# Kernel optimization log

Measured on AMD Instinct MI355X. Metric: run time of the kernel, lower is better.

## Reference

```python
import jax, jax.numpy as jnp
import numpy as np

C = 1024
H = 16
DH = C // H
DFF = 4 * C
D = 1024  # cond_dim
B = 2
L = 2048
MAX_SCALE_MUL = float(np.log(100.0))
EPS = 1e-6


def _ln(x):
    # LayerNorm without affine, eps=1e-6
    m = jnp.mean(x, axis=-1, keepdims=True)
    xc = x - m
    var = jnp.mean(xc * xc, axis=-1, keepdims=True)
    return xc * jax.lax.rsqrt(var + EPS)


def setup_inputs() -> dict:
    key = jax.random.key(0)
    ks = jax.random.split(key, 16)
    s = 0.02
    return {
        "x": jax.random.normal(ks[0], (B, L, C), jnp.float32),
        "cond_BD": jax.random.normal(ks[1], (B, D), jnp.float32),
        "attn_bias": jax.random.normal(ks[2], (1, 1, L, L), jnp.float32) * 0.1,
        "qkv_w": jax.random.normal(ks[3], (3 * C, C), jnp.float32) * s,
        "q_bias": jnp.zeros((C,), jnp.float32),
        "v_bias": jnp.zeros((C,), jnp.float32),
        "scale_mul": jnp.full((1, H, 1, 1), np.log(4.0), jnp.float32),
        "proj_w": jax.random.normal(ks[4], (C, C), jnp.float32) * s,
        "proj_b": jnp.zeros((C,), jnp.float32),
        "fc1_w": jax.random.normal(ks[5], (DFF, C), jnp.float32) * s,
        "fc1_b": jnp.zeros((DFF,), jnp.float32),
        "fc2_w": jax.random.normal(ks[6], (C, DFF), jnp.float32) * s,
        "fc2_b": jnp.zeros((C,), jnp.float32),
        "ada_w": jax.random.normal(ks[7], (6 * C, D), jnp.float32) * s,
        "ada_b": jnp.zeros((6 * C,), jnp.float32),
    }


def _attention(x, attn_bias, qkv_w, q_bias, v_bias, scale_mul, proj_w, proj_b):
    b, l, c = x.shape
    bias = jnp.concatenate([q_bias, jnp.zeros_like(q_bias), v_bias])
    qkv = x @ qkv_w.T + bias  # [B,L,3C]
    qkv = qkv.reshape(b, l, 3, H, DH).transpose(2, 0, 3, 1, 4)  # [3,B,H,L,DH]
    q, k, v = qkv[0], qkv[1], qkv[2]
    sm = jnp.exp(jnp.minimum(scale_mul, MAX_SCALE_MUL))  # [1,H,1,1]
    q = q * jax.lax.rsqrt(jnp.sum(q * q, -1, keepdims=True).clip(1e-24)) * sm
    k = k * jax.lax.rsqrt(jnp.sum(k * k, -1, keepdims=True).clip(1e-24))
    attn = jnp.einsum("bhqd,bhkd->bhqk", q, k) + attn_bias
    attn = jax.nn.softmax(attn, axis=-1)
    out = jnp.einsum("bhqk,bhkd->bhqd", attn, v)
    out = out.transpose(0, 2, 1, 3).reshape(b, l, c)
    return out @ proj_w.T + proj_b


def reference(x, cond_BD, attn_bias, qkv_w, q_bias, v_bias, scale_mul,
              proj_w, proj_b, fc1_w, fc1_b, fc2_w, fc2_b, ada_w, ada_b):
    # adaLN modulation: SiLU -> Linear -> 6 chunks of C
    ada = jax.nn.silu(cond_BD) @ ada_w.T + ada_b  # [B,6C]
    ada = ada.reshape(-1, 1, 6, C)
    g1, g2, s1, s2, sh1, sh2 = [ada[:, :, i, :] for i in range(6)]  # each [B,1,C]
    # attention branch
    h = _ln(x) * (s1 + 1.0) + sh1
    x = x + _attention(h, attn_bias, qkv_w, q_bias, v_bias, scale_mul, proj_w, proj_b) * g1
    # FFN branch (GELU tanh approx)
    h = _ln(x) * (s2 + 1.0) + sh2
    h = jax.nn.gelu(h @ fc1_w.T + fc1_b, approximate=True) @ fc2_w.T + fc2_b
    x = x + h * g2
    return x
```

## Files before the change

kernel.cpp:

```cpp
#include <hip/hip_runtime.h>
#include <stdint.h>

#define Ll 2048
#define Mrows 4096

typedef unsigned short u16;
typedef __attribute__((ext_vector_type(8))) short short8;
typedef __attribute__((ext_vector_type(4))) float f32x4;

__device__ __forceinline__ float b2f(u16 b) {
  union { float f; unsigned u; } x; x.u = ((unsigned)b) << 16; return x.f;
}
__device__ __forceinline__ u16 f2b(float v) {
  union { float f; unsigned u; } x; x.f = v;
  unsigned r = x.u + 0x7fffu + ((x.u >> 16) & 1u);
  return (u16)(r >> 16);
}

#define GLOAD_LDS16(gp, sp)                                                        \
  __builtin_amdgcn_global_load_lds(                                                \
      (__attribute__((address_space(1))) void*)(void*)(gp),                        \
      (__attribute__((address_space(3))) void*)(sp), 16, 0, 0)

__global__ __launch_bounds__(256) void k_f32_to_bf16(const float* __restrict__ src,
                                                     u16* __restrict__ dst) {
  const int i = blockIdx.x * 256 + threadIdx.x;
  const float4 v = ((const float4*)src)[i];
  ushort4 o;
  o.x = f2b(v.x); o.y = f2b(v.y); o.z = f2b(v.z); o.w = f2b(v.w);
  ((ushort4*)dst)[i] = o;
}

__global__ void k_qkvbias(const float* __restrict__ qb, const float* __restrict__ vb,
                          float* __restrict__ out) {
  const int i = blockIdx.x * 256 + threadIdx.x;
  out[i] = (i < 1024) ? qb[i] : (i < 2048 ? 0.f : vb[i - 2048]);
}

__global__ __launch_bounds__(256) void k_ada(const float* __restrict__ cond,
                                             const float* __restrict__ aw,
                                             const float* __restrict__ ab,
                                             float* __restrict__ out) {
  const int wv = threadIdx.x >> 6, lane = threadIdx.x & 63;
  const int j = blockIdx.x * 4 + wv;
  const int b = j / 6144, jj = j % 6144;
  const float* wr = aw + (size_t)jj * 1024;
  const float* cr = cond + b * 1024;
  float acc = 0.f;
  for (int d = lane; d < 1024; d += 64) {
    const float cv = cr[d];
    acc += (cv / (1.f + __expf(-cv))) * wr[d];
  }
  for (int off = 32; off; off >>= 1) acc += __shfl_xor(acc, off);
  if (lane == 0) out[b * 6144 + jj] = acc + ab[jj];
}

__global__ __launch_bounds__(256) void k_ln_mod(const float* __restrict__ x,
                                                const float* __restrict__ ada,
                                                u16* __restrict__ out,
                                                int s_off, int sh_off) {
  const int row = blockIdx.x;
  const int b = row >> 11;
  const int t = threadIdx.x;
  const float4 xv = ((const float4*)(x + (size_t)row * 1024))[t];
  float s = xv.x + xv.y + xv.z + xv.w;
  float s2 = xv.x * xv.x + xv.y * xv.y + xv.z * xv.z + xv.w * xv.w;
  for (int off = 32; off; off >>= 1) { s += __shfl_xor(s, off); s2 += __shfl_xor(s2, off); }
  __shared__ float red[8];
  const int wv = t >> 6, lane = t & 63;
  if (lane == 0) { red[wv] = s; red[4 + wv] = s2; }
  __syncthreads();
  s = red[0] + red[1] + red[2] + red[3];
  s2 = red[4] + red[5] + red[6] + red[7];
  const float mean = s * (1.f / 1024.f);
  const float var = s2 * (1.f / 1024.f) - mean * mean;
  const float rstd = rsqrtf(var + 1e-6f);
  const float4 sv = ((const float4*)(ada + b * 6144 + s_off))[t];
  const float4 shv = ((const float4*)(ada + b * 6144 + sh_off))[t];
  ushort4 ov;
  ov.x = f2b((xv.x - mean) * rstd * (1.f + sv.x) + shv.x);
  ov.y = f2b((xv.y - mean) * rstd * (1.f + sv.y) + shv.y);
  ov.z = f2b((xv.z - mean) * rstd * (1.f + sv.z) + shv.z);
  ov.w = f2b((xv.w - mean) * rstd * (1.f + sv.w) + shv.w);
  ((ushort4*)(out + (size_t)row * 1024))[t] = ov;
}

__global__ __launch_bounds__(256) void k_resid_ln(const float* __restrict__ x,
                                                  const float* __restrict__ p,
                                                  const float* __restrict__ ada,
                                                  float* __restrict__ x2,
                                                  u16* __restrict__ out) {
  const int row = blockIdx.x;
  const int b = row >> 11;
  const int t = threadIdx.x;
  const float4 xv = ((const float4*)(x + (size_t)row * 1024))[t];
  const float4 pv = ((const float4*)(p + (size_t)row * 1024))[t];
  const float4 gv = ((const float4*)(ada + b * 6144 + 0))[t];
  float4 v;
  v.x = xv.x + pv.x * gv.x; v.y = xv.y + pv.y * gv.y;
  v.z = xv.z + pv.z * gv.z; v.w = xv.w + pv.w * gv.w;
  ((float4*)(x2 + (size_t)row * 1024))[t] = v;
  float s = v.x + v.y + v.z + v.w;
  float s2 = v.x * v.x + v.y * v.y + v.z * v.z + v.w * v.w;
  for (int off = 32; off; off >>= 1) { s += __shfl_xor(s, off); s2 += __shfl_xor(s2, off); }
  __shared__ float red[8];
  const int wv = t >> 6, lane = t & 63;
  if (lane == 0) { red[wv] = s; red[4 + wv] = s2; }
  __syncthreads();
  s = red[0] + red[1] + red[2] + red[3];
  s2 = red[4] + red[5] + red[6] + red[7];
  const float mean = s * (1.f / 1024.f);
  const float var = s2 * (1.f / 1024.f) - mean * mean;
  const float rstd = rsqrtf(var + 1e-6f);
  const float4 sv = ((const float4*)(ada + b * 6144 + 3072))[t];
  const float4 shv = ((const float4*)(ada + b * 6144 + 5120))[t];
  ushort4 ov;
  ov.x = f2b((v.x - mean) * rstd * (1.f + sv.x) + shv.x);
  ov.y = f2b((v.y - mean) * rstd * (1.f + sv.y) + shv.y);
  ov.z = f2b((v.z - mean) * rstd * (1.f + sv.z) + shv.z);
  ov.w = f2b((v.w - mean) * rstd * (1.f + sv.w) + shv.w);
  ((ushort4*)(out + (size_t)row * 1024))[t] = ov;
}

__global__ __launch_bounds__(256) void k_final(const float* __restrict__ x2,
                                               const float* __restrict__ f,
                                               const float* __restrict__ ada,
                                               float* __restrict__ out) {
  const int i = blockIdx.x * 256 + threadIdx.x;
  const int elem = i * 4;
  const int b = elem >> 21;
  const int c = elem & 1023;
  const float4 xv = ((const float4*)x2)[i];
  const float4 fv = ((const float4*)f)[i];
  const float4 gv = *(const float4*)(ada + b * 6144 + 1024 + c);
  float4 ov;
  ov.x = xv.x + fv.x * gv.x; ov.y = xv.y + fv.y * gv.y;
  ov.z = xv.z + fv.z * gv.z; ov.w = xv.w + fv.w * gv.w;
  ((float4*)out)[i] = ov;
}

__global__ __launch_bounds__(256) void k_qknorm(u16* __restrict__ qkv,
                                                const float* __restrict__ scale_mul) {
  const int wv = threadIdx.x >> 6, lane = threadIdx.x & 63;
  const int item = blockIdx.x * 4 + wv;
  const int h = item & 15;
  const int bl = item >> 4;
  const size_t base = (size_t)bl * 3072 + h * 64;
  const float q = b2f(qkv[base + lane]);
  float ss = q * q;
  for (int off = 32; off; off >>= 1) ss += __shfl_xor(ss, off);
  const float sm = __expf(fminf(scale_mul[h], 4.605170185988091f));
  qkv[base + lane] = f2b(q * rsqrtf(fmaxf(ss, 1e-24f)) * sm);
  const float k = b2f(qkv[base + 1024 + lane]);
  ss = k * k;
  for (int off = 32; off; off >>= 1) ss += __shfl_xor(ss, off);
  qkv[base + 1024 + lane] = f2b(k * rsqrtf(fmaxf(ss, 1e-24f)));
}

template <int OUT_BF16, int GELU_ACT>
__global__ __launch_bounds__(256, 2)
void k_gemm_bt(const u16* __restrict__ A, const u16* __restrict__ W,
               const float* __restrict__ bias, void* __restrict__ Cout,
               int M, int N, int K) {
  __shared__ u16 As[128 * 64];
  __shared__ u16 Bs[128 * 64];
  const int tid = threadIdx.x;
  const int wv = tid >> 6;
  const int lane = tid & 63;
  const int q = lane >> 4;
  const int r = lane & 15;
  const int wm = (wv & 1) * 64;
  const int wn = (wv >> 1) * 64;
  const int m0 = blockIdx.x * 128;
  const int n0 = blockIdx.y * 128;

  f32x4 acc[4][4];
#pragma unroll
  for (int i = 0; i < 4; ++i)
#pragma unroll
    for (int j = 0; j < 4; ++j) acc[i][j] = (f32x4)0.0f;

  const int srow = tid >> 3;
  const int scol = (tid & 7) * 8;
  const u16* Ag = A + (size_t)(m0 + srow) * K + scol;
  const u16* Wg = W + (size_t)(n0 + srow) * K + scol;
  u16* AsBase = &As[wv * 512];
  u16* BsBase = &Bs[wv * 512];

  for (int kt = 0; kt < K; kt += 64) {
    __syncthreads();
#pragma unroll
    for (int p = 0; p < 4; ++p) {
      GLOAD_LDS16(Ag + (size_t)(p * 32) * K + kt, AsBase + p * 2048);
      GLOAD_LDS16(Wg + (size_t)(p * 32) * K + kt, BsBase + p * 2048);
    }
    __syncthreads();
#pragma unroll
    for (int kc = 0; kc < 2; ++kc) {
      short8 af[4], bfr[4];
#pragma unroll
      for (int i = 0; i < 4; ++i) {
        af[i] = *(const short8*)(As + (wm + i * 16 + r) * 64 + kc * 32 + q * 8);
        bfr[i] = *(const short8*)(Bs + (wn + i * 16 + r) * 64 + kc * 32 + q * 8);
      }
#pragma unroll
      for (int mi = 0; mi < 4; ++mi)
#pragma unroll
        for (int ni = 0; ni < 4; ++ni)
          acc[mi][ni] = __builtin_amdgcn_mfma_f32_16x16x32_bf16(af[mi], bfr[ni],
                                                                acc[mi][ni], 0, 0, 0);
    }
  }
#pragma unroll
  for (int mi = 0; mi < 4; ++mi) {
#pragma unroll
    for (int ni = 0; ni < 4; ++ni) {
      const int col = n0 + wn + ni * 16 + r;
      const float bv = bias[col];
#pragma unroll
      for (int rr = 0; rr < 4; ++rr) {
        const int rowg = m0 + wm + mi * 16 + q * 4 + rr;
        float v = acc[mi][ni][rr] + bv;
        if (GELU_ACT) {
          const float t = tanhf(0.7978845608028654f * (v + 0.044715f * v * v * v));
          v = 0.5f * v * (1.0f + t);
        }
        if (OUT_BF16)
          ((u16*)Cout)[(size_t)rowg * N + col] = f2b(v);
        else
          ((float*)Cout)[(size_t)rowg * N + col] = v;
      }
    }
  }
}

__global__ __launch_bounds__(256)
void k_flash(const u16* __restrict__ qkv, const u16* __restrict__ bias16,
             const float* __restrict__ scale_mul, u16* __restrict__ o) {
  __shared__ u16 Qs[64 * 64];
  __shared__ u16 Ks[64 * 64];
  __shared__ u16 Vt[64 * 72];
  __shared__ u16 Ps[4][16 * 64];
  __shared__ float stat[4][16];
  const int tid = threadIdx.x;
  const int bh = blockIdx.x;
  const int qb = blockIdx.y;
  const int b = bh >> 4, h = bh & 15;
  const int wv = tid >> 6, lane = tid & 63;
  const int quad = lane >> 4, c = lane & 15;
  const u16* Qg = qkv + (size_t)b * Ll * 3072 + h * 64;
  const u16* Kg = Qg + 1024;
  const u16* Vg = Qg + 2048;
  const float FMAX = __expf(fminf(scale_mul[h], 4.605170185988091f)) + 1.0f;

  {
    const int srow = tid >> 3, scol = (tid & 7) * 8;
    const u16* gp = Qg + (size_t)(qb * 64 + srow) * 3072 + scol;
    u16* lp = &Qs[wv * 512];
    GLOAD_LDS16(gp, lp);
    GLOAD_LDS16(gp + (size_t)32 * 3072, lp + 2048);
  }

  const int vc = tid & 15, va = (tid >> 4) & 1, vd0 = (tid >> 5) * 8;

  f32x4 S[4], O[4];
  float lacc[4];
#pragma unroll
  for (int i = 0; i < 4; ++i) { O[i] = (f32x4)0.f; lacc[i] = 0.f; }
  const u16* brow = bias16 + (size_t)(qb * 64 + wv * 16 + quad * 4) * 2048;

  for (int kt = 0; kt < 32; ++kt) {
    __syncthreads();
    {
      const int srow = tid >> 3, scol = (tid & 7) * 8;
      const u16* gp = Kg + (size_t)(kt * 64 + srow) * 3072 + scol;
      u16* lp = &Ks[wv * 512];
      GLOAD_LDS16(gp, lp);
      GLOAD_LDS16(gp + (size_t)32 * 3072, lp + 2048);
    }
    {
      union { uint4 v; u16 s[8]; } r0, r1;
      const u16* vp = Vg + (size_t)(kt * 64 + vc + 32 * va) * 3072 + vd0;
      r0.v = *(const uint4*)vp;
      r1.v = *(const uint4*)(vp + (size_t)16 * 3072);
#pragma unroll
      for (int j = 0; j < 8; ++j)
        *(unsigned*)(&Vt[(vd0 + j) * 72 + vc * 4 + va * 2]) =
            (unsigned)r0.s[j] | ((unsigned)r1.s[j] << 16);
    }
    __syncthreads();

    u16 bv[4][4];
#pragma unroll
    for (int rr = 0; rr < 4; ++rr)
#pragma unroll
      for (int ni = 0; ni < 4; ++ni)
        bv[rr][ni] = brow[rr * 2048 + kt * 64 + ni * 16 + c];

#pragma unroll
    for (int i = 0; i < 4; ++i) S[i] = (f32x4)0.f;
#pragma unroll
    for (int ks = 0; ks < 2; ++ks) {
      const short8 aq = *(const short8*)(&Qs[(wv * 16 + c) * 64 + ks * 32 + quad * 8]);
#pragma unroll
      for (int ni = 0; ni < 4; ++ni) {
        const short8 bk = *(const short8*)(&Ks[(ni * 16 + c) * 64 + ks * 32 + quad * 8]);
        S[ni] = __builtin_amdgcn_mfma_f32_16x16x32_bf16(aq, bk, S[ni], 0, 0, 0);
      }
    }

#pragma unroll
    for (int rr = 0; rr < 4; ++rr) {
      const float p0 = __expf(S[0][rr] + b2f(bv[rr][0]) - FMAX);
      const float p1 = __expf(S[1][rr] + b2f(bv[rr][1]) - FMAX);
      const float p2 = __expf(S[2][rr] + b2f(bv[rr][2]) - FMAX);
      const float p3 = __expf(S[3][rr] + b2f(bv[rr][3]) - FMAX);
      lacc[rr] += (p0 + p1) + (p2 + p3);
      ushort4 pk;
      pk.x = f2b(p0); pk.y = f2b(p1); pk.z = f2b(p2); pk.w = f2b(p3);
      *(ushort4*)(&Ps[wv][(quad * 4 + rr) * 64 + c * 4]) = pk;
    }
    __threadfence_block();
#pragma unroll
    for (int ks = 0; ks < 2; ++ks) {
      const short8 bp = *(const short8*)(&Ps[wv][c * 64 + ks * 32 + quad * 8]);
#pragma unroll
      for (int i = 0; i < 4; ++i) {
        const short8 av = *(const short8*)(&Vt[(i * 16 + c) * 72 + ks * 32 + quad * 8]);
        O[i] = __builtin_amdgcn_mfma_f32_16x16x32_bf16(av, bp, O[i], 0, 0, 0);
      }
    }
  }

#pragma unroll
  for (int rr = 0; rr < 4; ++rr) {
    float l = lacc[rr];
    l += __shfl_xor(l, 1); l += __shfl_xor(l, 2);
    l += __shfl_xor(l, 4); l += __shfl_xor(l, 8);
    lacc[rr] = l;
  }
  if (c == 0)
    *(float4*)(&stat[wv][quad * 4]) = make_float4(lacc[0], lacc[1], lacc[2], lacc[3]);
  __threadfence_block();
  const float inv = 1.f / stat[wv][c];
  u16* op = o + (size_t)(b * Ll + qb * 64 + wv * 16 + c) * 1024 + h * 64;
#pragma unroll
  for (int i = 0; i < 4; ++i) {
    ushort4 ov;
    ov.x = f2b(O[i][0] * inv); ov.y = f2b(O[i][1] * inv);
    ov.z = f2b(O[i][2] * inv); ov.w = f2b(O[i][3] * inv);
    *(ushort4*)(op + i * 16 + quad * 4) = ov;
  }
}

extern "C" void kernel_launch(void* const* d_in, const int* in_sizes, int n_in,
                              void* d_out, int out_size, void* d_ws, size_t ws_size,
                              hipStream_t stream) {
  const float* x = (const float*)d_in[0];
  const float* cond = (const float*)d_in[1];
  const float* attn_bias = (const float*)d_in[2];
  const float* qkv_w = (const float*)d_in[3];
  const float* q_bias = (const float*)d_in[4];
  const float* v_bias = (const float*)d_in[5];
  const float* scale_mul = (const float*)d_in[6];
  const float* proj_w = (const float*)d_in[7];
  const float* proj_b = (const float*)d_in[8];
  const float* fc1_w = (const float*)d_in[9];
  const float* fc1_b = (const float*)d_in[10];
  const float* fc2_w = (const float*)d_in[11];
  const float* fc2_b = (const float*)d_in[12];
  const float* ada_w = (const float*)d_in[13];
  const float* ada_b = (const float*)d_in[14];
  float* out = (float*)d_out;
  char* ws = (char*)d_ws;

  float* ada_out = (float*)(ws + 0);
  float* qkv_bias = (float*)(ws + 49152);
  u16* wqkv = (u16*)(ws + 61440);
  u16* wproj = (u16*)(ws + 6352896);
  u16* wfc1 = (u16*)(ws + 8450048);
  u16* wfc2 = (u16*)(ws + 16838656);
  u16* sb = (u16*)(ws + 25227264);
  u16* big = (u16*)(ws + 33615872);
  float* g32 = (float*)(ws + 67170304);
  float* x2 = (float*)(ws + 83947520);
  u16* wbias = big + (size_t)4096 * 3072;

  k_f32_to_bf16<<<3072, 256, 0, stream>>>(qkv_w, wqkv);
  k_f32_to_bf16<<<1024, 256, 0, stream>>>(proj_w, wproj);
  k_f32_to_bf16<<<4096, 256, 0, stream>>>(fc1_w, wfc1);
  k_f32_to_bf16<<<4096, 256, 0, stream>>>(fc2_w, wfc2);
  k_f32_to_bf16<<<4096, 256, 0, stream>>>(attn_bias, wbias);
  k_qkvbias<<<12, 256, 0, stream>>>(q_bias, v_bias, qkv_bias);
  k_ada<<<3072, 256, 0, stream>>>(cond, ada_w, ada_b, ada_out);
  k_ln_mod<<<4096, 256, 0, stream>>>(x, ada_out, sb, 2048, 4096);
  k_gemm_bt<1, 0><<<dim3(32, 24), 256, 0, stream>>>(sb, wqkv, qkv_bias, big,
                                                    Mrows, 3072, 1024);
  k_qknorm<<<16384, 256, 0, stream>>>(big, scale_mul);
  k_flash<<<dim3(32, 32), 256, 0, stream>>>(big, wbias, scale_mul, sb);
  k_gemm_bt<0, 0><<<dim3(32, 8), 256, 0, stream>>>(sb, wproj, proj_b, g32,
                                                   Mrows, 1024, 1024);
  k_resid_ln<<<4096, 256, 0, stream>>>(x, g32, ada_out, x2, sb);
  k_gemm_bt<1, 1><<<dim3(32, 32), 256, 0, stream>>>(sb, wfc1, fc1_b, big,
                                                    Mrows, 4096, 1024);
  k_gemm_bt<0, 0><<<dim3(32, 8), 256, 0, stream>>>(big, wfc2, fc2_b, g32,
                                                   Mrows, 1024, 4096);
  k_final<<<4096, 256, 0, stream>>>(x2, g32, ada_out, out);
}
```

Before: 514.4 us.

## Split-K the narrow GEMMs, fuse QK-norm into QKV GEMM, merge conversions

The proj and fc2 GEMMs (N=1024, 256 tiles) now use two-way split-K over gridDim.z. This raises the tile count to 512 so the CUs are better filled, and the two partial outputs are summed inside the residual/LN and final kernels. A dedicated QKV GEMM applies the q/v bias, the per-head L2 normalisation and the scale in its epilogue using intra-quad shuffles, removing the separate qknorm pass over the QKV buffer. The five weight/bias conversions become one kernel launch, and the qkv_bias kernel is dropped. In exchange, each split-K GEMM writes an extra fp32 partial buffer, which adds memory traffic, and workspace regions are reused for those partials.

```diff
diff --git a/kernel.cpp b/kernel.cpp
--- a/kernel.cpp
+++ b/kernel.cpp
@@ -22,19 +22,24 @@
       (__attribute__((address_space(1))) void*)(void*)(gp),                        \
       (__attribute__((address_space(3))) void*)(sp), 16, 0, 0)
 
-__global__ __launch_bounds__(256) void k_f32_to_bf16(const float* __restrict__ src,
-                                                     u16* __restrict__ dst) {
-  const int i = blockIdx.x * 256 + threadIdx.x;
-  const float4 v = ((const float4*)src)[i];
+__global__ __launch_bounds__(256) void k_convert_all(
+    const float* __restrict__ s0, u16* __restrict__ d0,
+    const float* __restrict__ s1, u16* __restrict__ d1,
+    const float* __restrict__ s2, u16* __restrict__ d2,
+    const float* __restrict__ s3, u16* __restrict__ d3,
+    const float* __restrict__ s4, u16* __restrict__ d4) {
+  int i = blockIdx.x * 256 + threadIdx.x;
+  const float* s; u16* d; int off;
+  if (i < 786432)       { s = s0; d = d0; off = 0; }
+  else if (i < 1048576) { s = s1; d = d1; off = 786432; }
+  else if (i < 2097152) { s = s2; d = d2; off = 1048576; }
+  else if (i < 3145728) { s = s3; d = d3; off = 2097152; }
+  else                  { s = s4; d = d4; off = 3145728; }
+  i -= off;
+  const float4 v = ((const float4*)s)[i];
   ushort4 o;
   o.x = f2b(v.x); o.y = f2b(v.y); o.z = f2b(v.z); o.w = f2b(v.w);
-  ((ushort4*)dst)[i] = o;
-}
-
-__global__ void k_qkvbias(const float* __restrict__ qb, const float* __restrict__ vb,
-                          float* __restrict__ out) {
-  const int i = blockIdx.x * 256 + threadIdx.x;
-  out[i] = (i < 1024) ? qb[i] : (i < 2048 ? 0.f : vb[i - 2048]);
+  ((ushort4*)d)[i] = o;
 }
 
 __global__ __launch_bounds__(256) void k_ada(const float* __restrict__ cond,
@@ -86,7 +91,8 @@
 }
 
 __global__ __launch_bounds__(256) void k_resid_ln(const float* __restrict__ x,
-                                                  const float* __restrict__ p,
+                                                  const float* __restrict__ p0,
+                                                  const float* __restrict__ p1,
                                                   const float* __restrict__ ada,
                                                   float* __restrict__ x2,
                                                   u16* __restrict__ out) {
@@ -94,11 +100,12 @@
   const int b = row >> 11;
   const int t = threadIdx.x;
   const float4 xv = ((const float4*)(x + (size_t)row * 1024))[t];
-  const float4 pv = ((const float4*)(p + (size_t)row * 1024))[t];
+  const float4 pa = ((const float4*)(p0 + (size_t)row * 1024))[t];
+  const float4 pb = ((const float4*)(p1 + (size_t)row * 1024))[t];
   const float4 gv = ((const float4*)(ada + b * 6144 + 0))[t];
   float4 v;
-  v.x = xv.x + pv.x * gv.x; v.y = xv.y + pv.y * gv.y;
-  v.z = xv.z + pv.z * gv.z; v.w = xv.w + pv.w * gv.w;
+  v.x = xv.x + (pa.x + pb.x) * gv.x; v.y = xv.y + (pa.y + pb.y) * gv.y;
+  v.z = xv.z + (pa.z + pb.z) * gv.z; v.w = xv.w + (pa.w + pb.w) * gv.w;
   ((float4*)(x2 + (size_t)row * 1024))[t] = v;
   float s = v.x + v.y + v.z + v.w;
   float s2 = v.x * v.x + v.y * v.y + v.z * v.z + v.w * v.w;
@@ -123,7 +130,8 @@
 }
 
 __global__ __launch_bounds__(256) void k_final(const float* __restrict__ x2,
-                                               const float* __restrict__ f,
+                                               const float* __restrict__ f0,
+                                               const float* __restrict__ f1,
                                                const float* __restrict__ ada,
                                                float* __restrict__ out) {
   const int i = blockIdx.x * 256 + threadIdx.x;
@@ -131,37 +139,20 @@
   const int b = elem >> 21;
   const int c = elem & 1023;
   const float4 xv = ((const float4*)x2)[i];
-  const float4 fv = ((const float4*)f)[i];
+  const float4 fa = ((const float4*)f0)[i];
+  const float4 fb = ((const float4*)f1)[i];
   const float4 gv = *(const float4*)(ada + b * 6144 + 1024 + c);
   float4 ov;
-  ov.x = xv.x + fv.x * gv.x; ov.y = xv.y + fv.y * gv.y;
-  ov.z = xv.z + fv.z * gv.z; ov.w = xv.w + fv.w * gv.w;
+  ov.x = xv.x + (fa.x + fb.x) * gv.x; ov.y = xv.y + (fa.y + fb.y) * gv.y;
+  ov.z = xv.z + (fa.z + fb.z) * gv.z; ov.w = xv.w + (fa.w + fb.w) * gv.w;
   ((float4*)out)[i] = ov;
-}
-
-__global__ __launch_bounds__(256) void k_qknorm(u16* __restrict__ qkv,
-                                                const float* __restrict__ scale_mul) {
-  const int wv = threadIdx.x >> 6, lane = threadIdx.x & 63;
-  const int item = blockIdx.x * 4 + wv;
-  const int h = item & 15;
-  const int bl = item >> 4;
-  const size_t base = (size_t)bl * 3072 + h * 64;
-  const float q = b2f(qkv[base + lane]);
-  float ss = q * q;
-  for (int off = 32; off; off >>= 1) ss += __shfl_xor(ss, off);
-  const float sm = __expf(fminf(scale_mul[h], 4.605170185988091f));
-  qkv[base + lane] = f2b(q * rsqrtf(fmaxf(ss, 1e-24f)) * sm);
-  const float k = b2f(qkv[base + 1024 + lane]);
-  ss = k * k;
-  for (int off = 32; off; off >>= 1) ss += __shfl_xor(ss, off);
-  qkv[base + 1024 + lane] = f2b(k * rsqrtf(fmaxf(ss, 1e-24f)));
 }
 
 template <int OUT_BF16, int GELU_ACT>
 __global__ __launch_bounds__(256, 2)
 void k_gemm_bt(const u16* __restrict__ A, const u16* __restrict__ W,
                const float* __restrict__ bias, void* __restrict__ Cout,
-               int M, int N, int K) {
+               float* __restrict__ Cout2, int M, int N, int Kc) {
   __shared__ u16 As[128 * 64];
   __shared__ u16 Bs[128 * 64];
   const int tid = threadIdx.x;
@@ -173,6 +164,8 @@
   const int wn = (wv >> 1) * 64;
   const int m0 = blockIdx.x * 128;
   const int n0 = blockIdx.y * 128;
+  const int K = Kc * gridDim.z;
+  const int kt0 = blockIdx.z * Kc;
 
   f32x4 acc[4][4];
 #pragma unroll
@@ -187,7 +180,7 @@
   u16* AsBase = &As[wv * 512];
   u16* BsBase = &Bs[wv * 512];
 
-  for (int kt = 0; kt < K; kt += 64) {
+  for (int kt = kt0; kt < kt0 + Kc; kt += 64) {
     __syncthreads();
 #pragma unroll
     for (int p = 0; p < 4; ++p) {
@@ -211,12 +204,13 @@
                                                                 acc[mi][ni], 0, 0, 0);
     }
   }
+  float* Cf = (blockIdx.z == 0) ? (float*)Cout : Cout2;
 #pragma unroll
   for (int mi = 0; mi < 4; ++mi) {
 #pragma unroll
     for (int ni = 0; ni < 4; ++ni) {
       const int col = n0 + wn + ni * 16 + r;
-      const float bv = bias[col];
+      const float bv = (blockIdx.z == 0) ? bias[col] : 0.f;
 #pragma unroll
       for (int rr = 0; rr < 4; ++rr) {
         const int rowg = m0 + wm + mi * 16 + q * 4 + rr;
@@ -228,7 +222,100 @@
         if (OUT_BF16)
           ((u16*)Cout)[(size_t)rowg * N + col] = f2b(v);
         else
-          ((float*)Cout)[(size_t)rowg * N + col] = v;
+          Cf[(size_t)rowg * N + col] = v;
+      }
+    }
+  }
+}
+
+__global__ __launch_bounds__(256, 2)
+void k_gemm_qkv(const u16* __restrict__ A, const u16* __restrict__ W,
+                const float* __restrict__ qb, const float* __restrict__ vb,
+                const float* __restrict__ scale_mul, u16* __restrict__ Cout) {
+  const int N = 3072, K = 1024;
+  __shared__ u16 As[128 * 64];
+  __shared__ u16 Bs[128 * 64];
+  const int tid = threadIdx.x;
+  const int wv = tid >> 6;
+  const int lane = tid & 63;
+  const int q = lane >> 4;
+  const int r = lane & 15;
+  const int wm = (wv & 1) * 64;
+  const int wn = (wv >> 1) * 64;
+  const int m0 = blockIdx.x * 128;
+  const int n0 = blockIdx.y * 128;
+
+  f32x4 acc[4][4];
+#pragma unroll
+  for (int i = 0; i < 4; ++i)
+#pragma unroll
+    for (int j = 0; j < 4; ++j) acc[i][j] = (f32x4)0.0f;
+
+  const int srow = tid >> 3;
+  const int scol = (tid & 7) * 8;
+  const u16* Ag = A + (size_t)(m0 + srow) * K + scol;
+  const u16* Wg = W + (size_t)(n0 + srow) * K + scol;
+  u16* AsBase = &As[wv * 512];
+  u16* BsBase = &Bs[wv * 512];
+
+  for (int kt = 0; kt < K; kt += 64) {
+    __syncthreads();
+#pragma unroll
+    for (int p = 0; p < 4; ++p) {
+      GLOAD_LDS16(Ag + (size_t)(p * 32) * K + kt, AsBase + p * 2048);
+      GLOAD_LDS16(Wg + (size_t)(p * 32) * K + kt, BsBase + p * 2048);
+    }
+    __syncthreads();
+#pragma unroll
+    for (int kc = 0; kc < 2; ++kc) {
+      short8 af[4], bfr[4];
+#pragma unroll
+      for (int i = 0; i < 4; ++i) {
+        af[i] = *(const short8*)(As + (wm + i * 16 + r) * 64 + kc * 32 + q * 8);
+        bfr[i] = *(const short8*)(Bs + (wn + i * 16 + r) * 64 + kc * 32 + q * 8);
+      }
+#pragma unroll
+      for (int mi = 0; mi < 4; ++mi)
+#pragma unroll
+        for (int ni = 0; ni < 4; ++ni)
+          acc[mi][ni] = __builtin_amdgcn_mfma_f32_16x16x32_bf16(af[mi], bfr[ni],
+                                                                acc[mi][ni], 0, 0, 0);
+    }
+  }
+  const int cb = n0 + wn;
+  const int sec = cb >> 10;
+  const int hh = (cb >> 6) & 15;
+  const float sm = (sec == 0) ? __expf(fminf(scale_mul[hh], 4.605170185988091f)) : 1.f;
+#pragma unroll
+  for (int mi = 0; mi < 4; ++mi) {
+    float v[4][4];
+#pragma unroll
+    for (int ni = 0; ni < 4; ++ni) {
+      const int d = ni * 16 + r;
+      const float bvv = (sec == 0) ? qb[(cb & 1023) + d]
+                        : (sec == 2 ? vb[(cb & 1023) + d] : 0.f);
+#pragma unroll
+      for (int rr = 0; rr < 4; ++rr) v[ni][rr] = acc[mi][ni][rr] + bvv;
+    }
+    if (sec < 2) {
+#pragma unroll
+      for (int rr = 0; rr < 4; ++rr) {
+        float ss = v[0][rr] * v[0][rr] + v[1][rr] * v[1][rr] +
+                   v[2][rr] * v[2][rr] + v[3][rr] * v[3][rr];
+        ss += __shfl_xor(ss, 1); ss += __shfl_xor(ss, 2);
+        ss += __shfl_xor(ss, 4); ss += __shfl_xor(ss, 8);
+        const float sc = rsqrtf(fmaxf(ss, 1e-24f)) * sm;
+#pragma unroll
+        for (int ni = 0; ni < 4; ++ni) v[ni][rr] *= sc;
+      }
+    }
+#pragma unroll
+    for (int ni = 0; ni < 4; ++ni) {
+      const int col = cb + ni * 16 + r;
+#pragma unroll
+      for (int rr = 0; rr < 4; ++rr) {
+        const int rowg = m0 + wm + mi * 16 + q * 4 + rr;
+        Cout[(size_t)rowg * N + col] = f2b(v[ni][rr]);
       }
     }
   }
@@ -375,7 +462,6 @@
   char* ws = (char*)d_ws;
 
   float* ada_out = (float*)(ws + 0);
-  float* qkv_bias = (float*)(ws + 49152);
   u16* wqkv = (u16*)(ws + 61440);
   u16* wproj = (u16*)(ws + 6352896);
   u16* wfc1 = (u16*)(ws + 8450048);
@@ -385,25 +471,24 @@
   float* g32 = (float*)(ws + 67170304);
   float* x2 = (float*)(ws + 83947520);
   u16* wbias = big + (size_t)4096 * 3072;
-
-  k_f32_to_bf16<<<3072, 256, 0, stream>>>(qkv_w, wqkv);
-  k_f32_to_bf16<<<1024, 256, 0, stream>>>(proj_w, wproj);
-  k_f32_to_bf16<<<4096, 256, 0, stream>>>(fc1_w, wfc1);
-  k_f32_to_bf16<<<4096, 256, 0, stream>>>(fc2_w, wfc2);
-  k_f32_to_bf16<<<4096, 256, 0, stream>>>(attn_bias, wbias);
-  k_qkvbias<<<12, 256, 0, stream>>>(q_bias, v_bias, qkv_bias);
+  float* projp0 = (float*)big;
+  float* projp1 = (float*)(big + (size_t)8 * 1024 * 1024);
+  float* fc2p1 = (float*)(ws + 61440);
+
+  k_convert_all<<<16384, 256, 0, stream>>>(qkv_w, wqkv, proj_w, wproj,
+                                           fc1_w, wfc1, fc2_w, wfc2,
+                                           attn_bias, wbias);
   k_ada<<<3072, 256, 0, stream>>>(cond, ada_w, ada_b, ada_out);
   k_ln_mod<<<4096, 256, 0, stream>>>(x, ada_out, sb, 2048, 4096);
-  k_gemm_bt<1, 0><<<dim3(32, 24), 256, 0, stream>>>(sb, wqkv, qkv_bias, big,
-                                                    Mrows, 3072, 1024);
-  k_qknorm<<<16384, 256, 0, stream>>>(big, scale_mul);
+  k_gemm_qkv<<<dim3(32, 24), 256, 0, stream>>>(sb, wqkv, q_bias, v_bias,
+                                               scale_mul, big);
   k_flash<<<dim3(32, 32), 256, 0, stream>>>(big, wbias, scale_mul, sb);
-  k_gemm_bt<0, 0><<<dim3(32, 8), 256, 0, stream>>>(sb, wproj, proj_b, g32,
-                                                   Mrows, 1024, 1024);
-  k_resid_ln<<<4096, 256, 0, stream>>>(x, g32, ada_out, x2, sb);
-  k_gemm_bt<1, 1><<<dim3(32, 32), 256, 0, stream>>>(sb, wfc1, fc1_b, big,
-                                                    Mrows, 4096, 1024);
-  k_gemm_bt<0, 0><<<dim3(32, 8), 256, 0, stream>>>(big, wfc2, fc2_b, g32,
-                                                   Mrows, 1024, 4096);
-  k_final<<<4096, 256, 0, stream>>>(x2, g32, ada_out, out);
-}
+  k_gemm_bt<0, 0><<<dim3(32, 8, 2), 256, 0, stream>>>(sb, wproj, proj_b, projp0,
+                                                      projp1, Mrows, 1024, 512);
+  k_resid_ln<<<4096, 256, 0, stream>>>(x, projp0, projp1, ada_out, x2, sb);
+  k_gemm_bt<1, 1><<<dim3(32, 32, 1), 256, 0, stream>>>(sb, wfc1, fc1_b, big,
+                                                       nullptr, Mrows, 4096, 1024);
+  k_gemm_bt<0, 0><<<dim3(32, 8, 2), 256, 0, stream>>>(big, wfc2, fc2_b, g32,
+                                                      fc2p1, Mrows, 1024, 2048);
+  k_final<<<4096, 256, 0, stream>>>(x2, g32, fc2p1, ada_out, out);
+}
```

Measured after the change: 451.5 us. 1.14x faster.
